# Performance work log

Measured on AMD Instinct MI355X. Metric: run time of the kernel, lower is better.

The kernel has to match this reference:

```python
import jax, jax.numpy as jnp
import numpy as np

B, S, E, H = 4, 2048, 1024, 16
D = E // H  # head_size = 64

def setup_inputs() -> dict:
    key = jax.random.key(0)
    k1, k2, k3 = jax.random.split(key, 3)
    x = jax.random.normal(k1, (B, S, E), dtype=jnp.float32)
    # torch Linear weight is (out,in); we store transposed (in,out) for x @ W
    w_attn = jax.random.normal(k2, (E, 3 * E), dtype=jnp.float32) * (1.0 / np.sqrt(E))
    w_proj = jax.random.normal(k3, (E, E), dtype=jnp.float32) * (1.0 / np.sqrt(E))
    return {"x": x, "w_attn": w_attn, "w_proj": w_proj}

def reference(x, w_attn, w_proj):
    b, s, e = x.shape
    qkv = x @ w_attn                      # (B,S,3E)
    q, k, v = jnp.split(qkv, 3, axis=2)
    # (B,S,H,D) -> (B,H,S,D)
    q = q.reshape(b, s, H, D).transpose(0, 2, 1, 3)
    k = k.reshape(b, s, H, D).transpose(0, 2, 1, 3)
    v = v.reshape(b, s, H, D).transpose(0, 2, 1, 3)
    scale = 1.0 / np.sqrt(D).astype(np.float32)
    att = jnp.einsum('bhqd,bhkd->bhqk', q, k) * scale  # (B,H,S,S)
    causal = jnp.tril(jnp.ones((s, s), dtype=bool))
    att = jnp.where(causal[None, None, :, :], att, jnp.float32(-jnp.inf))
    att = jax.nn.softmax(att, axis=-1)
    # dropout layers are identity in eval mode
    y = jnp.einsum('bhqk,bhkd->bhqd', att, v)          # (B,H,S,D)
    y = y.transpose(0, 2, 1, 3).reshape(b, s, e)       # (B,S,E)
    return y @ w_proj
```

## Files before the change

kernel.cpp:

```cpp
#include <hip/hip_runtime.h>
#include <hip/hip_bf16.h>
#include <cstdint>

typedef __attribute__((ext_vector_type(8))) short bf16x8;
typedef __attribute__((ext_vector_type(4))) short short4v;
typedef __attribute__((ext_vector_type(4))) float f32x4;

#define MFMA(a, b, c) __builtin_amdgcn_mfma_f32_16x16x32_bf16((a), (b), (c), 0, 0, 0)

__device__ __forceinline__ unsigned short f2bf(float f) {
  union { float f; unsigned int u; } v;
  v.f = f;
  unsigned int r = v.u + 0x7FFFu + ((v.u >> 16) & 1u);
  return (unsigned short)(r >> 16);
}

__device__ __forceinline__ unsigned short f2bf_ru(float f) {
  union { float f; unsigned int u; } v;
  v.f = f;
  return (unsigned short)((v.u + 0x8000u) >> 16);
}

__device__ __forceinline__ void async_cp16(const unsigned short* g, unsigned short* l) {
  __builtin_amdgcn_global_load_lds(
      (const __attribute__((address_space(1))) unsigned int*)g,
      (__attribute__((address_space(3))) unsigned int*)l, 16, 0, 0);
}

__global__ __launch_bounds__(256) void cvt_x(const float* __restrict__ in,
                                             unsigned short* __restrict__ out) {
  size_t i = ((size_t)blockIdx.x * 256 + threadIdx.x) * 8;
  float4 a = *(const float4*)(in + i);
  float4 b = *(const float4*)(in + i + 4);
  bf16x8 p;
  p[0] = (short)f2bf(a.x); p[1] = (short)f2bf(a.y);
  p[2] = (short)f2bf(a.z); p[3] = (short)f2bf(a.w);
  p[4] = (short)f2bf(b.x); p[5] = (short)f2bf(b.y);
  p[6] = (short)f2bf(b.z); p[7] = (short)f2bf(b.w);
  *(bf16x8*)(out + i) = p;
}

__global__ __launch_bounds__(256) void transpose_cvt(const float* __restrict__ in,
                                                     unsigned short* __restrict__ out,
                                                     int K, int N) {
  __shared__ float tile[64][65];
  int k0 = blockIdx.x * 64;
  int n0 = blockIdx.y * 64;
  int c = threadIdx.x & 63;
  int rb = threadIdx.x >> 6;
#pragma unroll
  for (int i = 0; i < 16; ++i) {
    int r = rb * 16 + i;
    tile[r][c] = in[(size_t)(k0 + r) * N + (n0 + c)];
  }
  __syncthreads();
#pragma unroll
  for (int i = 0; i < 16; ++i) {
    int r = rb * 16 + i;
    out[(size_t)(n0 + r) * K + (k0 + c)] = f2bf(tile[c][r]);
  }
}

__global__ __launch_bounds__(256) void gemm_qkv(const unsigned short* __restrict__ X,
                                                const unsigned short* __restrict__ WT,
                                                unsigned short* __restrict__ qb,
                                                unsigned short* __restrict__ kb,
                                                unsigned short* __restrict__ vt) {
  const int K = 1024;
  __shared__ unsigned short As[128 * 64];
  __shared__ unsigned short Bs[128 * 64];
  int t = threadIdx.x, lane = t & 63, w = t >> 6;
  int quad = lane >> 4, l15 = lane & 15;
  int sl7 = l15 & 7;
  int wm = (w >> 1) * 64, wn = (w & 1) * 64;
  int row0 = blockIdx.y * 128, col0 = blockIdx.x * 128;
  int srow = w * 8 + (lane >> 3);
  int schunk = (lane & 7) ^ (lane >> 3);
  const unsigned short* aSrc = X + (size_t)(row0 + srow) * K + schunk * 8;
  const unsigned short* bSrc = WT + (size_t)(col0 + srow) * K + schunk * 8;
  unsigned short* ldsA = &As[(w * 8) * 64];
  unsigned short* ldsB = &Bs[(w * 8) * 64];
  f32x4 zero4 = {0.f, 0.f, 0.f, 0.f};
  f32x4 acc[4][4];
#pragma unroll
  for (int i = 0; i < 4; ++i)
#pragma unroll
    for (int j = 0; j < 4; ++j) acc[i][j] = zero4;

  for (int k0 = 0; k0 < K; k0 += 64) {
    __syncthreads();
#pragma unroll
    for (int i = 0; i < 4; ++i)
      async_cp16(aSrc + (size_t)i * 32 * K + k0, ldsA + i * 32 * 64);
#pragma unroll
    for (int i = 0; i < 4; ++i)
      async_cp16(bSrc + (size_t)i * 32 * K + k0, ldsB + i * 32 * 64);
    __syncthreads();
#pragma unroll
    for (int h = 0; h < 2; ++h) {
      bf16x8 af[4], bfr[4];
#pragma unroll
      for (int mt = 0; mt < 4; ++mt)
        af[mt] = *(const bf16x8*)&As[(wm + mt * 16 + l15) * 64 +
                                     ((h * 4 + quad) ^ sl7) * 8];
#pragma unroll
      for (int nt = 0; nt < 4; ++nt)
        bfr[nt] = *(const bf16x8*)&Bs[(wn + nt * 16 + l15) * 64 +
                                      ((h * 4 + quad) ^ sl7) * 8];
#pragma unroll
      for (int mt = 0; mt < 4; ++mt)
#pragma unroll
        for (int nt = 0; nt < 4; ++nt)
          acc[mt][nt] = MFMA(af[mt], bfr[nt], acc[mt][nt]);
    }
  }

  const float qscale = 0.125f * 1.4426950408889634f;
#pragma unroll
  for (int mt = 0; mt < 4; ++mt) {
    int rix0 = row0 + wm + mt * 16 + quad * 4;
    int b = rix0 >> 11;
    int s0 = rix0 & 2047;
#pragma unroll
    for (int nt = 0; nt < 4; ++nt) {
      int c = col0 + wn + nt * 16 + l15;
      int which = c >> 10;
      int e = c & 1023;
      int h = e >> 6, d = e & 63;
      size_t bh = (size_t)b * 16 + h;
      if (which == 2) {
        short4v pv;
#pragma unroll
        for (int r = 0; r < 4; ++r) pv[r] = (short)f2bf(acc[mt][nt][r]);
        *(short4v*)(vt + (bh * 64 + d) * 2048 + s0) = pv;
      } else {
        unsigned short* dst = (which == 0) ? qb : kb;
        float sc = (which == 0) ? qscale : 1.0f;
#pragma unroll
        for (int r = 0; r < 4; ++r)
          dst[(bh * 2048 + (s0 + r)) * 64 + d] = f2bf(acc[mt][nt][r] * sc);
      }
    }
  }
}

__global__ __launch_bounds__(256, 2) void flash_attn(const unsigned short* __restrict__ qb,
                                                     const unsigned short* __restrict__ kb,
                                                     const unsigned short* __restrict__ vt,
                                                     unsigned short* __restrict__ yb) {
  __shared__ unsigned short Ks[64 * 68];
  __shared__ unsigned short P[4][16 * 68];
  int idx = blockIdx.x;
  int bh = idx & 63;
  int p = idx >> 6;
  int t = threadIdx.x, lane = t & 63, w = t >> 6;
  int quad = lane >> 4, l15 = lane & 15;
  unsigned short* Pw = P[w];
  f32x4 zero4 = {0.f, 0.f, 0.f, 0.f};
  bf16x8 ones;
#pragma unroll
  for (int i = 0; i < 8; ++i) ones[i] = (short)0x3F80;

  int srow = t >> 2;
  int sseg = (t & 3) * 8;
  const unsigned short* Kg = kb + ((size_t)bh * 2048 + srow) * 64 + sseg;
  int b = bh >> 4, h = bh & 15;

  for (int seg = 0; seg < 2; ++seg) {
    int qt = seg ? p : (15 - p);
    int qrow0 = qt * 128 + w * 32;
    int ktmax = 2 * qt + 1;

    bf16x8 aq0[2], aq1[2];
#pragma unroll
    for (int s = 0; s < 2; ++s) {
      const unsigned short* Qp =
          qb + ((size_t)bh * 2048 + qrow0 + s * 16 + l15) * 64 + quad * 8;
      aq0[s] = *(const bf16x8*)Qp;
      aq1[s] = *(const bf16x8*)(Qp + 32);
    }
    f32x4 o[2][4], accl[2];
#pragma unroll
    for (int s = 0; s < 2; ++s) {
      accl[s] = zero4;
#pragma unroll
      for (int nt = 0; nt < 4; ++nt) o[s][nt] = zero4;
    }

    bf16x8 kg0 = *(const bf16x8*)Kg;
    bf16x8 kg1 = *(const bf16x8*)(Kg + 32);

    for (int kt = 0; kt <= ktmax; ++kt) {
      int kbase = kt * 64;
      __syncthreads();
      *(bf16x8*)&Ks[srow * 68 + sseg] = kg0;
      *(bf16x8*)&Ks[srow * 68 + sseg + 32] = kg1;
      __syncthreads();
      if (kt < ktmax) {
        const unsigned short* nk = Kg + (size_t)(kbase + 64) * 64;
        kg0 = *(const bf16x8*)nk;
        kg1 = *(const bf16x8*)(nk + 32);
      }
      if (kbase > qrow0 + 31) continue;

      bf16x8 vf0[4], vf1[4];
#pragma unroll
      for (int nt = 0; nt < 4; ++nt) {
        const unsigned short* Vp =
            vt + ((size_t)bh * 64 + nt * 16 + l15) * 2048 + kbase + quad * 8;
        vf0[nt] = *(const bf16x8*)Vp;
        vf1[nt] = *(const bf16x8*)(Vp + 32);
      }
      bf16x8 kf0[4], kf1[4];
#pragma unroll
      for (int nt = 0; nt < 4; ++nt) {
        kf0[nt] = *(const bf16x8*)&Ks[(nt * 16 + l15) * 68 + quad * 8];
        kf1[nt] = *(const bf16x8*)&Ks[(nt * 16 + l15) * 68 + 32 + quad * 8];
      }

#pragma unroll
      for (int s = 0; s < 2; ++s) {
        int rowb = qrow0 + s * 16;
        if (kbase > rowb + 15) continue;
        f32x4 sv[4];
#pragma unroll
        for (int nt = 0; nt < 4; ++nt) {
          f32x4 z = zero4;
          z = MFMA(aq0[s], kf0[nt], z);
          z = MFMA(aq1[s], kf1[nt], z);
          sv[nt] = z;
        }
        if (kbase + 63 > rowb) {
#pragma unroll
          for (int nt = 0; nt < 4; ++nt) {
            int col = kbase + nt * 16 + l15;
#pragma unroll
            for (int r = 0; r < 4; ++r)
              if (col > rowb + quad * 4 + r) sv[nt][r] = -1e30f;
          }
        }
#pragma unroll
        for (int nt = 0; nt < 4; ++nt)
#pragma unroll
          for (int r = 0; r < 4; ++r) {
            float pv = __builtin_amdgcn_exp2f(sv[nt][r]);
            Pw[(quad * 4 + r) * 68 + nt * 16 + l15] = f2bf_ru(pv);
          }
        bf16x8 ap0 = *(const bf16x8*)&Pw[l15 * 68 + quad * 8];
        bf16x8 ap1 = *(const bf16x8*)&Pw[l15 * 68 + 32 + quad * 8];
        accl[s] = MFMA(ap0, ones, accl[s]);
        accl[s] = MFMA(ap1, ones, accl[s]);
#pragma unroll
        for (int nt = 0; nt < 4; ++nt) {
          o[s][nt] = MFMA(ap0, vf0[nt], o[s][nt]);
          o[s][nt] = MFMA(ap1, vf1[nt], o[s][nt]);
        }
      }
    }

#pragma unroll
    for (int s = 0; s < 2; ++s) {
      float inv[4];
#pragma unroll
      for (int r = 0; r < 4; ++r) inv[r] = 1.0f / accl[s][r];
#pragma unroll
      for (int nt = 0; nt < 4; ++nt) {
        int e = h * 64 + nt * 16 + l15;
#pragma unroll
        for (int r = 0; r < 4; ++r) {
          int srow_g = qrow0 + s * 16 + quad * 4 + r;
          yb[((size_t)b * 2048 + srow_g) * 1024 + e] = f2bf(o[s][nt][r] * inv[r]);
        }
      }
    }
  }
}

__global__ __launch_bounds__(256) void gemm_proj(const unsigned short* __restrict__ Y,
                                                 const unsigned short* __restrict__ WT,
                                                 float* __restrict__ out) {
  const int K = 1024;
  __shared__ unsigned short As[128 * 64];
  __shared__ unsigned short Bs[128 * 64];
  int t = threadIdx.x, lane = t & 63, w = t >> 6;
  int quad = lane >> 4, l15 = lane & 15;
  int sl7 = l15 & 7;
  int wm = (w >> 1) * 64, wn = (w & 1) * 64;
  int row0 = blockIdx.y * 128, col0 = blockIdx.x * 128;
  int srow = w * 8 + (lane >> 3);
  int schunk = (lane & 7) ^ (lane >> 3);
  const unsigned short* aSrc = Y + (size_t)(row0 + srow) * K + schunk * 8;
  const unsigned short* bSrc = WT + (size_t)(col0 + srow) * K + schunk * 8;
  unsigned short* ldsA = &As[(w * 8) * 64];
  unsigned short* ldsB = &Bs[(w * 8) * 64];
  f32x4 zero4 = {0.f, 0.f, 0.f, 0.f};
  f32x4 acc[4][4];
#pragma unroll
  for (int i = 0; i < 4; ++i)
#pragma unroll
    for (int j = 0; j < 4; ++j) acc[i][j] = zero4;

  for (int k0 = 0; k0 < K; k0 += 64) {
    __syncthreads();
#pragma unroll
    for (int i = 0; i < 4; ++i)
      async_cp16(aSrc + (size_t)i * 32 * K + k0, ldsA + i * 32 * 64);
#pragma unroll
    for (int i = 0; i < 4; ++i)
      async_cp16(bSrc + (size_t)i * 32 * K + k0, ldsB + i * 32 * 64);
    __syncthreads();
#pragma unroll
    for (int h = 0; h < 2; ++h) {
      bf16x8 af[4], bfr[4];
#pragma unroll
      for (int mt = 0; mt < 4; ++mt)
        af[mt] = *(const bf16x8*)&As[(wm + mt * 16 + l15) * 64 +
                                     ((h * 4 + quad) ^ sl7) * 8];
#pragma unroll
      for (int nt = 0; nt < 4; ++nt)
        bfr[nt] = *(const bf16x8*)&Bs[(wn + nt * 16 + l15) * 64 +
                                      ((h * 4 + quad) ^ sl7) * 8];
#pragma unroll
      for (int mt = 0; mt < 4; ++mt)
#pragma unroll
        for (int nt = 0; nt < 4; ++nt)
          acc[mt][nt] = MFMA(af[mt], bfr[nt], acc[mt][nt]);
    }
  }

#pragma unroll
  for (int mt = 0; mt < 4; ++mt) {
    int rix0 = row0 + wm + mt * 16 + quad * 4;
#pragma unroll
    for (int nt = 0; nt < 4; ++nt) {
      int c = col0 + wn + nt * 16 + l15;
#pragma unroll
      for (int r = 0; r < 4; ++r)
        out[(size_t)(rix0 + r) * 1024 + c] = acc[mt][nt][r];
    }
  }
}

extern "C" void kernel_launch(void* const* d_in, const int* in_sizes, int n_in,
                              void* d_out, int out_size, void* d_ws, size_t ws_size,
                              hipStream_t stream) {
  const float* x = (const float*)d_in[0];
  const float* w_attn = (const float*)d_in[1];
  const float* w_proj = (const float*)d_in[2];
  float* out = (float*)d_out;
  char* ws = (char*)d_ws;
  unsigned short* wT  = (unsigned short*)(ws + 0);
  unsigned short* wpT = (unsigned short*)(ws + 6291456);
  unsigned short* qb  = (unsigned short*)(ws + 8388608);
  unsigned short* kb  = (unsigned short*)(ws + 25165824);
  unsigned short* vt  = (unsigned short*)(ws + 41943040);
  unsigned short* xyb = (unsigned short*)(ws + 58720256);

  cvt_x<<<4096, 256, 0, stream>>>(x, xyb);
  transpose_cvt<<<dim3(16, 48), 256, 0, stream>>>(w_attn, wT, 1024, 3072);
  transpose_cvt<<<dim3(16, 16), 256, 0, stream>>>(w_proj, wpT, 1024, 1024);
  gemm_qkv<<<dim3(24, 64), 256, 0, stream>>>(xyb, wT, qb, kb, vt);
  flash_attn<<<dim3(512), 256, 0, stream>>>(qb, kb, vt, xyb);
  gemm_proj<<<dim3(8, 64), 256, 0, stream>>>(xyb, wpT, out);
}
```

Measured before the change: 256.5 us.

## Halve flash-attention query tile, double grid, and group heads per XCD

The flash attention kernel now processes 64-row query tiles (16 rows per wave) instead of 128, launching 1024 blocks instead of 512 with a higher occupancy hint. Block indices are remapped so the same head's blocks land on one XCD for L2 reuse of K/V. Per-block register use drops, which allows more waves in flight. In exchange each K tile is loaded and staged in shared memory for half as many query rows.

```diff
diff --git a/kernel.cpp b/kernel.cpp
--- a/kernel.cpp
+++ b/kernel.cpp
@@ -144,15 +144,17 @@
   }
 }
 
-__global__ __launch_bounds__(256, 2) void flash_attn(const unsigned short* __restrict__ qb,
+__global__ __launch_bounds__(256, 4) void flash_attn(const unsigned short* __restrict__ qb,
                                                      const unsigned short* __restrict__ kb,
                                                      const unsigned short* __restrict__ vt,
                                                      unsigned short* __restrict__ yb) {
   __shared__ unsigned short Ks[64 * 68];
   __shared__ unsigned short P[4][16 * 68];
   int idx = blockIdx.x;
-  int bh = idx & 63;
-  int p = idx >> 6;
+  int xcd = idx & 7;
+  int local = idx >> 3;
+  int bh = xcd * 8 + (local & 7);
+  int p = local >> 3;
   int t = threadIdx.x, lane = t & 63, w = t >> 6;
   int quad = lane >> 4, l15 = lane & 15;
   unsigned short* Pw = P[w];
@@ -167,25 +169,18 @@
   int b = bh >> 4, h = bh & 15;
 
   for (int seg = 0; seg < 2; ++seg) {
-    int qt = seg ? p : (15 - p);
-    int qrow0 = qt * 128 + w * 32;
-    int ktmax = 2 * qt + 1;
-
-    bf16x8 aq0[2], aq1[2];
-#pragma unroll
-    for (int s = 0; s < 2; ++s) {
-      const unsigned short* Qp =
-          qb + ((size_t)bh * 2048 + qrow0 + s * 16 + l15) * 64 + quad * 8;
-      aq0[s] = *(const bf16x8*)Qp;
-      aq1[s] = *(const bf16x8*)(Qp + 32);
-    }
-    f32x4 o[2][4], accl[2];
-#pragma unroll
-    for (int s = 0; s < 2; ++s) {
-      accl[s] = zero4;
-#pragma unroll
-      for (int nt = 0; nt < 4; ++nt) o[s][nt] = zero4;
-    }
+    int qt = seg ? p : (31 - p);
+    int qrow0 = qt * 64 + w * 16;
+    int ktmax = qt;
+
+    const unsigned short* Qp = qb + ((size_t)bh * 2048 + qrow0 + l15) * 64 + quad * 8;
+    bf16x8 aq0 = *(const bf16x8*)Qp;
+    bf16x8 aq1 = *(const bf16x8*)(Qp + 32);
+
+    f32x4 o[4], accl;
+    accl = zero4;
+#pragma unroll
+    for (int nt = 0; nt < 4; ++nt) o[nt] = zero4;
 
     bf16x8 kg0 = *(const bf16x8*)Kg;
     bf16x8 kg1 = *(const bf16x8*)(Kg + 32);
@@ -201,7 +196,6 @@
         kg0 = *(const bf16x8*)nk;
         kg1 = *(const bf16x8*)(nk + 32);
       }
-      if (kbase > qrow0 + 31) continue;
 
       bf16x8 vf0[4], vf1[4];
 #pragma unroll
@@ -218,59 +212,51 @@
         kf1[nt] = *(const bf16x8*)&Ks[(nt * 16 + l15) * 68 + 32 + quad * 8];
       }
 
-#pragma unroll
-      for (int s = 0; s < 2; ++s) {
-        int rowb = qrow0 + s * 16;
-        if (kbase > rowb + 15) continue;
-        f32x4 sv[4];
+      f32x4 sv[4];
+#pragma unroll
+      for (int nt = 0; nt < 4; ++nt) {
+        f32x4 z = zero4;
+        z = MFMA(aq0, kf0[nt], z);
+        z = MFMA(aq1, kf1[nt], z);
+        sv[nt] = z;
+      }
+      if (kbase + 63 > qrow0) {
 #pragma unroll
         for (int nt = 0; nt < 4; ++nt) {
-          f32x4 z = zero4;
-          z = MFMA(aq0[s], kf0[nt], z);
-          z = MFMA(aq1[s], kf1[nt], z);
-          sv[nt] = z;
+          int col = kbase + nt * 16 + l15;
+#pragma unroll
+          for (int r = 0; r < 4; ++r)
+            if (col > qrow0 + quad * 4 + r) sv[nt][r] = -1e30f;
         }
-        if (kbase + 63 > rowb) {
-#pragma unroll
-          for (int nt = 0; nt < 4; ++nt) {
-            int col = kbase + nt * 16 + l15;
-#pragma unroll
-            for (int r = 0; r < 4; ++r)
-              if (col > rowb + quad * 4 + r) sv[nt][r] = -1e30f;
-          }
+      }
+#pragma unroll
+      for (int nt = 0; nt < 4; ++nt)
+#pragma unroll
+        for (int r = 0; r < 4; ++r) {
+          float pv = __builtin_amdgcn_exp2f(sv[nt][r]);
+          Pw[(quad * 4 + r) * 68 + nt * 16 + l15] = f2bf_ru(pv);
         }
-#pragma unroll
-        for (int nt = 0; nt < 4; ++nt)
-#pragma unroll
-          for (int r = 0; r < 4; ++r) {
-            float pv = __builtin_amdgcn_exp2f(sv[nt][r]);
-            Pw[(quad * 4 + r) * 68 + nt * 16 + l15] = f2bf_ru(pv);
-          }
-        bf16x8 ap0 = *(const bf16x8*)&Pw[l15 * 68 + quad * 8];
-        bf16x8 ap1 = *(const bf16x8*)&Pw[l15 * 68 + 32 + quad * 8];
-        accl[s] = MFMA(ap0, ones, accl[s]);
-        accl[s] = MFMA(ap1, ones, accl[s]);
-#pragma unroll
-        for (int nt = 0; nt < 4; ++nt) {
-          o[s][nt] = MFMA(ap0, vf0[nt], o[s][nt]);
-          o[s][nt] = MFMA(ap1, vf1[nt], o[s][nt]);
-        }
-      }
-    }
-
-#pragma unroll
-    for (int s = 0; s < 2; ++s) {
-      float inv[4];
-#pragma unroll
-      for (int r = 0; r < 4; ++r) inv[r] = 1.0f / accl[s][r];
+      bf16x8 ap0 = *(const bf16x8*)&Pw[l15 * 68 + quad * 8];
+      bf16x8 ap1 = *(const bf16x8*)&Pw[l15 * 68 + 32 + quad * 8];
+      accl = MFMA(ap0, ones, accl);
+      accl = MFMA(ap1, ones, accl);
 #pragma unroll
       for (int nt = 0; nt < 4; ++nt) {
-        int e = h * 64 + nt * 16 + l15;
-#pragma unroll
-        for (int r = 0; r < 4; ++r) {
-          int srow_g = qrow0 + s * 16 + quad * 4 + r;
-          yb[((size_t)b * 2048 + srow_g) * 1024 + e] = f2bf(o[s][nt][r] * inv[r]);
-        }
+        o[nt] = MFMA(ap0, vf0[nt], o[nt]);
+        o[nt] = MFMA(ap1, vf1[nt], o[nt]);
+      }
+    }
+
+    float inv[4];
+#pragma unroll
+    for (int r = 0; r < 4; ++r) inv[r] = 1.0f / accl[r];
+#pragma unroll
+    for (int nt = 0; nt < 4; ++nt) {
+      int e = h * 64 + nt * 16 + l15;
+#pragma unroll
+      for (int r = 0; r < 4; ++r) {
+        int srow_g = qrow0 + quad * 4 + r;
+        yb[((size_t)b * 2048 + srow_g) * 1024 + e] = f2bf(o[nt][r] * inv[r]);
       }
     }
   }
@@ -360,6 +346,6 @@
   transpose_cvt<<<dim3(16, 48), 256, 0, stream>>>(w_attn, wT, 1024, 3072);
   transpose_cvt<<<dim3(16, 16), 256, 0, stream>>>(w_proj, wpT, 1024, 1024);
   gemm_qkv<<<dim3(24, 64), 256, 0, stream>>>(xyb, wT, qb, kb, vt);
-  flash_attn<<<dim3(512), 256, 0, stream>>>(qb, kb, vt, xyb);
+  flash_attn<<<dim3(1024), 256, 0, stream>>>(qb, kb, vt, xyb);
   gemm_proj<<<dim3(8, 64), 256, 0, stream>>>(xyb, wpT, out);
 }
```

Result: slower. 310.4 us (+21.0%).

## Load K fragments directly from global with register double-buffering, drop LDS staging

Applied to the files above, without the earlier changes.

Removes the shared-memory staging of K tiles and the two block-wide barriers per key tile. Each wave now loads its own K fragments straight from global memory into a ping-pong pair of register buffers, prefetching the next tile while computing the current one. Each wave also stops at its own causal limit instead of the block-wide one. The block-to-head mapping is permuted so concurrently running blocks touch different batch/head groups. The cost is more global/L2 traffic, since every wave reloads K, and higher register pressure from the double buffers, which may reduce occupancy.

```diff
diff --git a/kernel.cpp b/kernel.cpp
--- a/kernel.cpp
+++ b/kernel.cpp
@@ -148,11 +148,11 @@
                                                      const unsigned short* __restrict__ kb,
                                                      const unsigned short* __restrict__ vt,
                                                      unsigned short* __restrict__ yb) {
-  __shared__ unsigned short Ks[64 * 68];
   __shared__ unsigned short P[4][16 * 68];
   int idx = blockIdx.x;
-  int bh = idx & 63;
   int p = idx >> 6;
+  int sub = idx & 63;
+  int bh = (sub & 7) * 8 + (sub >> 3);
   int t = threadIdx.x, lane = t & 63, w = t >> 6;
   int quad = lane >> 4, l15 = lane & 15;
   unsigned short* Pw = P[w];
@@ -160,16 +160,14 @@
   bf16x8 ones;
 #pragma unroll
   for (int i = 0; i < 8; ++i) ones[i] = (short)0x3F80;
-
-  int srow = t >> 2;
-  int sseg = (t & 3) * 8;
-  const unsigned short* Kg = kb + ((size_t)bh * 2048 + srow) * 64 + sseg;
   int b = bh >> 4, h = bh & 15;
+  const unsigned short* Kb = kb + (size_t)bh * (2048 * 64);
+  const unsigned short* Vb = vt + (size_t)bh * (64 * 2048);
 
   for (int seg = 0; seg < 2; ++seg) {
     int qt = seg ? p : (15 - p);
     int qrow0 = qt * 128 + w * 32;
-    int ktmax = 2 * qt + 1;
+    int ktmax = (qrow0 + 31) >> 6;
 
     bf16x8 aq0[2], aq1[2];
 #pragma unroll
@@ -187,76 +185,72 @@
       for (int nt = 0; nt < 4; ++nt) o[s][nt] = zero4;
     }
 
-    bf16x8 kg0 = *(const bf16x8*)Kg;
-    bf16x8 kg1 = *(const bf16x8*)(Kg + 32);
-
-    for (int kt = 0; kt <= ktmax; ++kt) {
-      int kbase = kt * 64;
-      __syncthreads();
-      *(bf16x8*)&Ks[srow * 68 + sseg] = kg0;
-      *(bf16x8*)&Ks[srow * 68 + sseg + 32] = kg1;
-      __syncthreads();
-      if (kt < ktmax) {
-        const unsigned short* nk = Kg + (size_t)(kbase + 64) * 64;
-        kg0 = *(const bf16x8*)nk;
-        kg1 = *(const bf16x8*)(nk + 32);
-      }
-      if (kbase > qrow0 + 31) continue;
-
-      bf16x8 vf0[4], vf1[4];
-#pragma unroll
-      for (int nt = 0; nt < 4; ++nt) {
-        const unsigned short* Vp =
-            vt + ((size_t)bh * 64 + nt * 16 + l15) * 2048 + kbase + quad * 8;
-        vf0[nt] = *(const bf16x8*)Vp;
-        vf1[nt] = *(const bf16x8*)(Vp + 32);
-      }
-      bf16x8 kf0[4], kf1[4];
-#pragma unroll
-      for (int nt = 0; nt < 4; ++nt) {
-        kf0[nt] = *(const bf16x8*)&Ks[(nt * 16 + l15) * 68 + quad * 8];
-        kf1[nt] = *(const bf16x8*)&Ks[(nt * 16 + l15) * 68 + 32 + quad * 8];
-      }
-
-#pragma unroll
-      for (int s = 0; s < 2; ++s) {
-        int rowb = qrow0 + s * 16;
-        if (kbase > rowb + 15) continue;
-        f32x4 sv[4];
-#pragma unroll
-        for (int nt = 0; nt < 4; ++nt) {
-          f32x4 z = zero4;
-          z = MFMA(aq0[s], kf0[nt], z);
-          z = MFMA(aq1[s], kf1[nt], z);
-          sv[nt] = z;
-        }
-        if (kbase + 63 > rowb) {
-#pragma unroll
-          for (int nt = 0; nt < 4; ++nt) {
-            int col = kbase + nt * 16 + l15;
-#pragma unroll
-            for (int r = 0; r < 4; ++r)
-              if (col > rowb + quad * 4 + r) sv[nt][r] = -1e30f;
-          }
-        }
-#pragma unroll
-        for (int nt = 0; nt < 4; ++nt)
-#pragma unroll
-          for (int r = 0; r < 4; ++r) {
-            float pv = __builtin_amdgcn_exp2f(sv[nt][r]);
-            Pw[(quad * 4 + r) * 68 + nt * 16 + l15] = f2bf_ru(pv);
-          }
-        bf16x8 ap0 = *(const bf16x8*)&Pw[l15 * 68 + quad * 8];
-        bf16x8 ap1 = *(const bf16x8*)&Pw[l15 * 68 + 32 + quad * 8];
-        accl[s] = MFMA(ap0, ones, accl[s]);
-        accl[s] = MFMA(ap1, ones, accl[s]);
-#pragma unroll
-        for (int nt = 0; nt < 4; ++nt) {
-          o[s][nt] = MFMA(ap0, vf0[nt], o[s][nt]);
-          o[s][nt] = MFMA(ap1, vf1[nt], o[s][nt]);
-        }
-      }
-    }
+    bf16x8 kA0[4], kA1[4], kB0[4], kB1[4];
+
+#define LOADK(kb0, k0, k1)                                                    \
+  do {                                                                        \
+    _Pragma("unroll") for (int nt = 0; nt < 4; ++nt) {                        \
+      const unsigned short* Kp =                                              \
+          Kb + (size_t)((kb0) + nt * 16 + l15) * 64 + quad * 8;               \
+      (k0)[nt] = *(const bf16x8*)Kp;                                          \
+      (k1)[nt] = *(const bf16x8*)(Kp + 32);                                   \
+    }                                                                         \
+  } while (0)
+
+#define COMPUTE(kbase_, k0, k1)                                               \
+  do {                                                                        \
+    int kbase = (kbase_);                                                     \
+    bf16x8 vf0[4], vf1[4];                                                    \
+    _Pragma("unroll") for (int nt = 0; nt < 4; ++nt) {                        \
+      const unsigned short* Vp =                                              \
+          Vb + (size_t)(nt * 16 + l15) * 2048 + kbase + quad * 8;             \
+      vf0[nt] = *(const bf16x8*)Vp;                                           \
+      vf1[nt] = *(const bf16x8*)(Vp + 32);                                    \
+    }                                                                         \
+    _Pragma("unroll") for (int s = 0; s < 2; ++s) {                           \
+      int rowb = qrow0 + s * 16;                                              \
+      if (kbase <= rowb + 15) {                             \
+        f32x4 sv[4];                                                          \
+        _Pragma("unroll") for (int nt = 0; nt < 4; ++nt) {                    \
+          f32x4 z = zero4;                                                    \
+          z = MFMA(aq0[s], (k0)[nt], z);                                      \
+          z = MFMA(aq1[s], (k1)[nt], z);                                      \
+          sv[nt] = z;                                                         \
+        }                                                                     \
+        if (kbase + 63 > rowb) {                \
+          _Pragma("unroll") for (int nt = 0; nt < 4; ++nt) {                  \
+            int col = kbase + nt * 16 + l15;                                  \
+            _Pragma("unroll") for (int r = 0; r < 4; ++r)                     \
+              if (col > rowb + quad * 4 + r) sv[nt][r] = -1e30f;              \
+          }                                                                   \
+        }                                                                     \
+        _Pragma("unroll") for (int nt = 0; nt < 4; ++nt)                      \
+          _Pragma("unroll") for (int r = 0; r < 4; ++r) {                     \
+            float pv = __builtin_amdgcn_exp2f(sv[nt][r]);                     \
+            Pw[(quad * 4 + r) * 68 + nt * 16 + l15] = f2bf_ru(pv);            \
+          }                                                                   \
+        bf16x8 ap0 = *(const bf16x8*)&Pw[l15 * 68 + quad * 8];                \
+        bf16x8 ap1 = *(const bf16x8*)&Pw[l15 * 68 + 32 + quad * 8];           \
+        accl[s] = MFMA(ap0, ones, accl[s]);                                   \
+        accl[s] = MFMA(ap1, ones, accl[s]);                                   \
+        _Pragma("unroll") for (int nt = 0; nt < 4; ++nt) {                    \
+          o[s][nt] = MFMA(ap0, vf0[nt], o[s][nt]);                            \
+          o[s][nt] = MFMA(ap1, vf1[nt], o[s][nt]);                            \
+        }                                                                     \
+      }                                                                       \
+    }                                                                         \
+  } while (0)
+
+    LOADK(0, kA0, kA1);
+    for (int kt = 0; kt <= ktmax; kt += 2) {
+      if (kt + 1 <= ktmax) LOADK((kt + 1) * 64, kB0, kB1);
+      COMPUTE(kt * 64, kA0, kA1);
+      if (kt + 1 > ktmax) break;
+      if (kt + 2 <= ktmax) LOADK((kt + 2) * 64, kA0, kA1);
+      COMPUTE((kt + 1) * 64, kB0, kB1);
+    }
+#undef LOADK
+#undef COMPUTE
 
 #pragma unroll
     for (int s = 0; s < 2; ++s) {
```

Result: slower. 302.7 us (+18.0%).

## Double-buffer K tiles via async global-to-LDS copies with swizzled layout

Applied to the files above, without the earlier changes.

The flash attention kernel now loads K tiles straight from global memory into a double-buffered LDS array using global_load_lds. The next tile is prefetched while the current one is used, and the loop needs one barrier per iteration instead of two. The padded LDS rows are replaced by an XOR-swizzled 64-wide layout to avoid bank conflicts without the padding. The block-to-head mapping is also permuted to change which heads run at the same time, likely for cache locality. The cost is twice the K LDS footprint, and correctness depends on the async copies being complete at the barrier.

```diff
diff --git a/kernel.cpp b/kernel.cpp
--- a/kernel.cpp
+++ b/kernel.cpp
@@ -148,11 +148,12 @@
                                                      const unsigned short* __restrict__ kb,
                                                      const unsigned short* __restrict__ vt,
                                                      unsigned short* __restrict__ yb) {
-  __shared__ unsigned short Ks[64 * 68];
+  __shared__ unsigned short Ks[2][64 * 64];
   __shared__ unsigned short P[4][16 * 68];
   int idx = blockIdx.x;
-  int bh = idx & 63;
   int p = idx >> 6;
+  int sub = idx & 63;
+  int bh = (sub & 7) * 8 + (sub >> 3);
   int t = threadIdx.x, lane = t & 63, w = t >> 6;
   int quad = lane >> 4, l15 = lane & 15;
   unsigned short* Pw = P[w];
@@ -160,11 +161,16 @@
   bf16x8 ones;
 #pragma unroll
   for (int i = 0; i < 8; ++i) ones[i] = (short)0x3F80;
-
-  int srow = t >> 2;
-  int sseg = (t & 3) * 8;
-  const unsigned short* Kg = kb + ((size_t)bh * 2048 + srow) * 64 + sseg;
   int b = bh >> 4, h = bh & 15;
+
+  int srow_st = t >> 3;
+  int sslot = (t & 7) ^ (srow_st & 7);
+  const unsigned short* kp0 =
+      kb + ((size_t)bh * 2048 + srow_st) * 64 + sslot * 8;
+  const unsigned short* kp1 = kp0 + 32 * 64;
+  const unsigned short* Vb = vt + (size_t)bh * (64 * 2048);
+  int rslot0 = (quad ^ (l15 & 7)) * 8;
+  int rslot1 = ((quad ^ 4) ^ (l15 & 7)) * 8;
 
   for (int seg = 0; seg < 2; ++seg) {
     int qt = seg ? p : (15 - p);
@@ -187,75 +193,77 @@
       for (int nt = 0; nt < 4; ++nt) o[s][nt] = zero4;
     }
 
-    bf16x8 kg0 = *(const bf16x8*)Kg;
-    bf16x8 kg1 = *(const bf16x8*)(Kg + 32);
+    __syncthreads();
+    async_cp16(kp0, &Ks[0][t * 8]);
+    async_cp16(kp1, &Ks[0][2048 + t * 8]);
+    int cur = 0;
 
     for (int kt = 0; kt <= ktmax; ++kt) {
       int kbase = kt * 64;
       __syncthreads();
-      *(bf16x8*)&Ks[srow * 68 + sseg] = kg0;
-      *(bf16x8*)&Ks[srow * 68 + sseg + 32] = kg1;
-      __syncthreads();
       if (kt < ktmax) {
-        const unsigned short* nk = Kg + (size_t)(kbase + 64) * 64;
-        kg0 = *(const bf16x8*)nk;
-        kg1 = *(const bf16x8*)(nk + 32);
+        const unsigned short* nk = kp0 + (size_t)(kbase + 64) * 64;
+        async_cp16(nk, &Ks[cur ^ 1][t * 8]);
+        async_cp16(nk + 32 * 64, &Ks[cur ^ 1][2048 + t * 8]);
       }
-      if (kbase > qrow0 + 31) continue;
-
-      bf16x8 vf0[4], vf1[4];
-#pragma unroll
-      for (int nt = 0; nt < 4; ++nt) {
-        const unsigned short* Vp =
-            vt + ((size_t)bh * 64 + nt * 16 + l15) * 2048 + kbase + quad * 8;
-        vf0[nt] = *(const bf16x8*)Vp;
-        vf1[nt] = *(const bf16x8*)(Vp + 32);
-      }
-      bf16x8 kf0[4], kf1[4];
-#pragma unroll
-      for (int nt = 0; nt < 4; ++nt) {
-        kf0[nt] = *(const bf16x8*)&Ks[(nt * 16 + l15) * 68 + quad * 8];
-        kf1[nt] = *(const bf16x8*)&Ks[(nt * 16 + l15) * 68 + 32 + quad * 8];
-      }
-
-#pragma unroll
-      for (int s = 0; s < 2; ++s) {
-        int rowb = qrow0 + s * 16;
-        if (kbase > rowb + 15) continue;
-        f32x4 sv[4];
+      if (kbase <= qrow0 + 31) {
+        const unsigned short* Kc = &Ks[cur][0];
+        bf16x8 vf0[4], vf1[4];
 #pragma unroll
         for (int nt = 0; nt < 4; ++nt) {
-          f32x4 z = zero4;
-          z = MFMA(aq0[s], kf0[nt], z);
-          z = MFMA(aq1[s], kf1[nt], z);
-          sv[nt] = z;
+          const unsigned short* Vp =
+              Vb + (size_t)(nt * 16 + l15) * 2048 + kbase + quad * 8;
+          vf0[nt] = *(const bf16x8*)Vp;
+          vf1[nt] = *(const bf16x8*)(Vp + 32);
         }
-        if (kbase + 63 > rowb) {
-#pragma unroll
-          for (int nt = 0; nt < 4; ++nt) {
-            int col = kbase + nt * 16 + l15;
-#pragma unroll
-            for (int r = 0; r < 4; ++r)
-              if (col > rowb + quad * 4 + r) sv[nt][r] = -1e30f;
+        bf16x8 kf0[4], kf1[4];
+#pragma unroll
+        for (int nt = 0; nt < 4; ++nt) {
+          kf0[nt] = *(const bf16x8*)&Kc[(nt * 16 + l15) * 64 + rslot0];
+          kf1[nt] = *(const bf16x8*)&Kc[(nt * 16 + l15) * 64 + rslot1];
+        }
+
+#pragma unroll
+        for (int s = 0; s < 2; ++s) {
+          int rowb = qrow0 + s * 16;
+          if (kbase <= rowb + 15) {
+            f32x4 sv[4];
+#pragma unroll
+            for (int nt = 0; nt < 4; ++nt) {
+              f32x4 z = zero4;
+              z = MFMA(aq0[s], kf0[nt], z);
+              z = MFMA(aq1[s], kf1[nt], z);
+              sv[nt] = z;
+            }
+            if (kbase + 63 > rowb) {
+#pragma unroll
+              for (int nt = 0; nt < 4; ++nt) {
+                int col = kbase + nt * 16 + l15;
+#pragma unroll
+                for (int r = 0; r < 4; ++r)
+                  if (col > rowb + quad * 4 + r) sv[nt][r] = -1e30f;
+              }
+            }
+#pragma unroll
+            for (int nt = 0; nt < 4; ++nt)
+#pragma unroll
+              for (int r = 0; r < 4; ++r) {
+                float pv = __builtin_amdgcn_exp2f(sv[nt][r]);
+                Pw[(quad * 4 + r) * 68 + nt * 16 + l15] = f2bf_ru(pv);
+              }
+            bf16x8 ap0 = *(const bf16x8*)&Pw[l15 * 68 + quad * 8];
+            bf16x8 ap1 = *(const bf16x8*)&Pw[l15 * 68 + 32 + quad * 8];
+            accl[s] = MFMA(ap0, ones, accl[s]);
+            accl[s] = MFMA(ap1, ones, accl[s]);
+#pragma unroll
+            for (int nt = 0; nt < 4; ++nt) {
+              o[s][nt] = MFMA(ap0, vf0[nt], o[s][nt]);
+              o[s][nt] = MFMA(ap1, vf1[nt], o[s][nt]);
+            }
           }
         }
-#pragma unroll
-        for (int nt = 0; nt < 4; ++nt)
-#pragma unroll
-          for (int r = 0; r < 4; ++r) {
-            float pv = __builtin_amdgcn_exp2f(sv[nt][r]);
-            Pw[(quad * 4 + r) * 68 + nt * 16 + l15] = f2bf_ru(pv);
-          }
-        bf16x8 ap0 = *(const bf16x8*)&Pw[l15 * 68 + quad * 8];
-        bf16x8 ap1 = *(const bf16x8*)&Pw[l15 * 68 + 32 + quad * 8];
-        accl[s] = MFMA(ap0, ones, accl[s]);
-        accl[s] = MFMA(ap1, ones, accl[s]);
-#pragma unroll
-        for (int nt = 0; nt < 4; ++nt) {
-          o[s][nt] = MFMA(ap0, vf0[nt], o[s][nt]);
-          o[s][nt] = MFMA(ap1, vf1[nt], o[s][nt]);
-        }
       }
+      cur ^= 1;
     }
 
 #pragma unroll
```

Measured after the change: 261.2 us. Within noise of the previous version (+1.8%).
